# Performance work log

Hardware: AMD Instinct MI355X
Metric: run time of the kernel (lower is better)

Reference implementation:

```python
import jax, jax.numpy as jnp
import numpy as np

KERNEL = 7  # median blur window size (odd)


def setup_inputs() -> dict:
    key = jax.random.key(0)
    # NCHW image batch, values in [0,1) like normalized images
    img = jax.random.uniform(key, (8, 3, 512, 512), dtype=jnp.float32)
    return {"img": img}


def _median_blur(img, k):
    # Matches kornia.filters.median_blur: zero padding ('same'), then median
    # over the k*k window. k*k is odd so the exact middle of the sorted
    # window equals torch.median's lower median.
    pad = k // 2
    b, c, h, w = img.shape
    x = jnp.pad(img, ((0, 0), (0, 0), (pad, pad), (pad, pad)))  # zero pad
    # unfold: [B, C, k*k, H, W] — same materialization as kornia's conv2d
    # with binary one-hot kernels. Loop is over the fixed k*k = 49 taps.
    patches = jnp.stack(
        [x[:, :, i:i + h, j:j + w] for i in range(k) for j in range(k)],
        axis=2,
    )
    mid = (k * k) // 2
    return jnp.sort(patches, axis=2)[:, :, mid]  # [B, C, H, W]


def reference(img):
    return _median_blur(img, KERNEL)
```

## Files before the change

kernel.cpp:

```cpp
#include <hip/hip_runtime.h>
#include <utility>

#define IMG_H 512
#define IMG_W 512

typedef _Float16 h2 __attribute__((ext_vector_type(2)));

__device__ __forceinline__ h2 h2min(h2 a, h2 b) { return __builtin_elementwise_min(a, b); }
__device__ __forceinline__ h2 h2max(h2 a, h2 b) { return __builtin_elementwise_max(a, b); }

struct Op { int kind, a, b; };
constexpr int NSLOT = 352;
constexpr int MAXOPS = 4096;
struct Prog { Op ops[MAXOPS]; int n; int nphys; bool ok; };

constexpr int pow2ceil(int x) { int p = 1; while (p < x) p += p; return p; }

struct Builder {
    Op ops[MAXOPS] = {};
    int n = 0;
    bool pad[NSLOT] = {};
    bool init[NSLOT] = {};
    bool ok = true;

    constexpr void emit(int k, int a, int b) {
        if (n < MAXOPS) ops[n++] = Op{k, a, b}; else ok = false;
    }
    constexpr void load(int s, int c) { emit(2, s, c); pad[s] = false; init[s] = true; }
    constexpr void mov(int d, int s) {
        if (!init[s] || d == s) ok = false;
        emit(1, d, s); pad[d] = pad[s]; init[d] = true;
    }
    constexpr void mkpad(int s) { pad[s] = true; init[s] = true; }
    constexpr void ce_(int a, int b) {
        if (!init[a] || !init[b]) { ok = false; return; }
        if (pad[a] && pad[b]) return;
        if (!pad[a] && pad[b]) return;
        if (pad[a] && !pad[b]) {
            emit(1, a, b); pad[a] = false; pad[b] = true; return;
        }
        emit(0, a, b);
    }
    constexpr void maxin(int a, int b) {
        if (!init[a] || !init[b] || pad[a] || pad[b]) ok = false;
        emit(5, a, b);
    }
    constexpr void minin(int a, int b) {
        if (!init[a] || !init[b] || pad[a] || pad[b]) ok = false;
        emit(4, a, b);
    }
    constexpr void sort_run(int base, int len) {
        for (int p = 1; p < len; p += p)
            for (int k = p; k > 0; k /= 2)
                for (int j = k % p; j + k < len; j += k + k)
                    for (int i = 0; i < k; ++i)
                        if (i + j + k < len)
                            if ((i + j) / (p + p) == (i + j + k) / (p + p))
                                ce_(base + i + j, base + i + j + k);
    }
    constexpr void merge_stage(int base, int P) {
        int nn = 2 * P, p = P;
        for (int k = p; k > 0; k /= 2)
            for (int j = k % p; j + k < nn; j += k + k)
                for (int i = 0; i < k; ++i) {
                    int a = i + j, b = i + j + k;
                    if (b < nn && a / (p + p) == b / (p + p)) ce_(base + a, base + b);
                }
    }
    constexpr void load_col(int base, int c) {
        for (int r = 0; r < 7; ++r) load(base + r, c * 7 + r);
        sort_run(base, 7);
    }
    constexpr void place(int dst, int src, int len, int P) {
        for (int i = 0; i < len; ++i) mov(dst + i, src + i);
        for (int i = len; i < P; ++i) mkpad(dst + i);
    }
    constexpr void merge_to(int dst, int s1, int l1, int s2, int l2) {
        int P = pow2ceil(l1 > l2 ? l1 : l2);
        place(dst, s1, l1, P);
        place(dst + P, s2, l2, P);
        merge_stage(dst, P);
    }
    constexpr void select_med49(int T, int A, int B, int o) {
        for (int t = 0; t < 7; ++t) {
            mov(T + t, A + 17 + t);
            maxin(B + 6 - t, T + t);
        }
        mov(T + 7, A + 24);
        minin(T, T + 1); minin(T + 2, T + 3);
        minin(T + 4, T + 5); minin(T + 6, T + 7);
        minin(T, T + 2); minin(T + 4, T + 6);
        minin(T, T + 4);
        if (!init[T] || pad[T]) ok = false;
        emit(3, o, T);
    }
};

constexpr Prog build() {
    Builder b{};
    constexpr int M12 = 112, M34 = 128, M56 = 144, M78 = 160, M910 = 176, M1112 = 192;
    constexpr int C28A = 208, C28B = 240, C42 = 272, T0 = 336, T1 = 344;

    for (int c = 1; c <= 8; ++c) b.load_col(8 * c, c);
    b.merge_to(M34, 8 * 3, 7, 8 * 4, 7);
    b.merge_to(M56, 8 * 5, 7, 8 * 6, 7);
    b.merge_to(C28A, M34, 14, M56, 14);
    b.merge_to(M12, 8 * 1, 7, 8 * 2, 7);
    b.merge_to(M78, 8 * 7, 7, 8 * 8, 7);

    b.merge_to(C42, C28A, 28, M12, 14);
    b.load_col(8 * 0, 0);
    b.select_med49(T0, C42, 8 * 0, 0);
    b.select_med49(T1, C42, 8 * 7, 1);

    b.merge_to(C42, C28A, 28, M78, 14);
    b.load_col(8 * 9, 9);
    b.select_med49(T0, C42, 8 * 2, 2);
    b.select_med49(T1, C42, 8 * 9, 3);

    b.load_col(8 * 10, 10);
    b.merge_to(M910, 8 * 9, 7, 8 * 10, 7);
    b.merge_to(C28B, M78, 14, M910, 14);

    b.merge_to(C42, C28B, 28, M56, 14);
    b.select_med49(T0, C42, 8 * 4, 4);
    b.load_col(8 * 11, 11);
    b.select_med49(T1, C42, 8 * 11, 5);

    b.load_col(8 * 12, 12);
    b.merge_to(M1112, 8 * 11, 7, 8 * 12, 7);
    b.merge_to(C42, C28B, 28, M1112, 14);
    b.select_med49(T0, C42, 8 * 6, 6);
    b.load_col(8 * 13, 13);
    b.select_med49(T1, C42, 8 * 13, 7);

    Prog p{};
    bool needed[NSLOT] = {};
    int kindr[MAXOPS] = {};
    bool keep[MAXOPS] = {};
    for (int t = b.n - 1; t >= 0; --t) {
        Op o = b.ops[t];
        if (o.kind == 3) { keep[t] = true; kindr[t] = 3; needed[o.b] = true; }
        else if (o.kind == 0) {
            bool na = needed[o.a], nb = needed[o.b];
            if (na && nb)      { keep[t] = true; kindr[t] = 0; }
            else if (na)       { keep[t] = true; kindr[t] = 4; needed[o.b] = true; }
            else if (nb)       { keep[t] = true; kindr[t] = 5; needed[o.a] = true; }
        } else if (o.kind == 1) {
            if (needed[o.a]) { keep[t] = true; kindr[t] = 1; needed[o.a] = false; needed[o.b] = true; }
        } else if (o.kind == 2) {
            if (needed[o.a]) { keep[t] = true; kindr[t] = 2; needed[o.a] = false; }
        } else if (o.kind == 4) {
            if (needed[o.a]) { keep[t] = true; kindr[t] = 4; needed[o.b] = true; }
        } else if (o.kind == 5) {
            if (needed[o.b]) { keep[t] = true; kindr[t] = 5; needed[o.a] = true; }
        }
    }
    p.n = 0;
    for (int t = 0; t < b.n; ++t)
        if (keep[t]) { p.ops[p.n] = b.ops[t]; p.ops[p.n].kind = kindr[t]; ++p.n; }
    p.ok = b.ok;

    bool live[NSLOT] = {};
    bool lu_a[MAXOPS] = {};
    bool lu_b[MAXOPS] = {};
    for (int t = p.n - 1; t >= 0; --t) {
        Op o = p.ops[t];
        if (o.kind == 0 || o.kind == 4 || o.kind == 5) {
            lu_a[t] = !live[o.a]; lu_b[t] = !live[o.b];
        } else if (o.kind == 1 || o.kind == 3) {
            lu_b[t] = !live[o.b];
        }
        if (o.kind == 0) { live[o.a] = false; live[o.b] = false; }
        else if (o.kind == 1 || o.kind == 2 || o.kind == 4) live[o.a] = false;
        else if (o.kind == 5) live[o.b] = false;
        if (o.kind == 0 || o.kind == 4 || o.kind == 5) { live[o.a] = true; live[o.b] = true; }
        else if (o.kind == 1 || o.kind == 3) live[o.b] = true;
    }
    for (int t = 0; t < p.n; ++t) {
        Op o = p.ops[t];
        if (o.kind == 0 && (lu_a[t] || lu_b[t])) p.ok = false;
        if (o.kind == 4 && lu_a[t]) p.ok = false;
        if (o.kind == 5 && lu_b[t]) p.ok = false;
    }
    int phys[NSLOT] = {};
    bool bound[NSLOT] = {};
    int freelist[NSLOT] = {};
    int nfree = 0, nphys = 0;
    for (int t = 0; t < p.n; ++t) {
        Op o = p.ops[t];
        if (o.kind == 0) {
            if (!bound[o.a] || !bound[o.b]) p.ok = false;
            p.ops[t].a = phys[o.a]; p.ops[t].b = phys[o.b];
        } else if (o.kind == 4) {
            if (!bound[o.a] || !bound[o.b]) p.ok = false;
            p.ops[t].a = phys[o.a]; p.ops[t].b = phys[o.b];
            if (lu_b[t]) { freelist[nfree++] = phys[o.b]; bound[o.b] = false; }
        } else if (o.kind == 5) {
            if (!bound[o.a] || !bound[o.b]) p.ok = false;
            p.ops[t].a = phys[o.a]; p.ops[t].b = phys[o.b];
            if (lu_a[t]) { freelist[nfree++] = phys[o.a]; bound[o.a] = false; }
        } else if (o.kind == 1) {
            if (!bound[o.b]) p.ok = false;
            int pb = phys[o.b];
            p.ops[t].b = pb;
            if (lu_b[t]) { freelist[nfree++] = pb; bound[o.b] = false; }
            if (bound[o.a]) { freelist[nfree++] = phys[o.a]; bound[o.a] = false; }
            int pa = (nfree > 0) ? freelist[--nfree] : nphys++;
            phys[o.a] = pa; bound[o.a] = true;
            p.ops[t].a = pa;
        } else if (o.kind == 2) {
            if (bound[o.a]) { freelist[nfree++] = phys[o.a]; bound[o.a] = false; }
            int pa = (nfree > 0) ? freelist[--nfree] : nphys++;
            phys[o.a] = pa; bound[o.a] = true;
            p.ops[t].a = pa;
        } else {
            if (!bound[o.b]) p.ok = false;
            p.ops[t].b = phys[o.b];
            if (lu_b[t]) { freelist[nfree++] = phys[o.b]; bound[o.b] = false; }
        }
        if (nphys > NSLOT || nfree > NSLOT) p.ok = false;
    }
    p.nphys = nphys;
    return p;
}

constexpr Prog PROG = build();
static_assert(PROG.ok && PROG.n > 0 && PROG.n < 2000, "program build failed");
static_assert(PROG.nphys > 0 && PROG.nphys <= 192, "regalloc blew up");

template <int P>
__device__ __forceinline__ h2& vslot(h2* v0, h2* v1, h2* v2) {
    if constexpr (P < 64) return v0[P];
    else if constexpr (P < 128) return v1[P - 64];
    else return v2[P - 128];
}
template <int P>
__device__ __forceinline__ h2 cslot(const h2* c0, const h2* c1) {
    if constexpr (P < 49) return c0[P];
    else return c1[P - 49];
}

template <int I>
__device__ __forceinline__ void step(h2* v0, h2* v1, h2* v2,
                                     const h2* c0, const h2* c1, h2* med) {
    constexpr Op o = PROG.ops[I];
    if constexpr (o.kind == 0) {
        h2& A = vslot<o.a>(v0, v1, v2);
        h2& B = vslot<o.b>(v0, v1, v2);
        h2 lo = h2min(A, B);
        h2 hi = h2max(A, B);
        A = lo; B = hi;
    } else if constexpr (o.kind == 1) {
        vslot<o.a>(v0, v1, v2) = vslot<o.b>(v0, v1, v2);
    } else if constexpr (o.kind == 2) {
        vslot<o.a>(v0, v1, v2) = cslot<o.b>(c0, c1);
    } else if constexpr (o.kind == 3) {
        med[o.a] = vslot<o.b>(v0, v1, v2);
    } else if constexpr (o.kind == 4) {
        h2& A = vslot<o.a>(v0, v1, v2);
        h2& B = vslot<o.b>(v0, v1, v2);
        A = h2min(A, B);
    } else {
        h2& A = vslot<o.a>(v0, v1, v2);
        h2& B = vslot<o.b>(v0, v1, v2);
        B = h2max(A, B);
    }
}

template <size_t... Is>
__device__ __forceinline__ void run_all(h2* v0, h2* v1, h2* v2,
                                        const h2* c0, const h2* c1, h2* med,
                                        std::index_sequence<Is...>) {
    (step<(int)Is>(v0, v1, v2, c0, c1, med), ...);
}

__global__ __launch_bounds__(256, 2) void median7x7_kernel(
        const float* __restrict__ img, float* __restrict__ out) {
    const int bc = blockIdx.z;
    const int tx = threadIdx.x;
    const int ty = threadIdx.y;
    const int x0 = (blockIdx.x * 64 + tx) * 8;
    const int y  = (blockIdx.y * 4 + ty) * 2;

    const float* base = img + (size_t)bc * (IMG_H * IMG_W);
    const bool okl = (x0 >= 4);
    const bool okr = (x0 <= 496);
    const int xl = okl ? (x0 - 4) : 0;
    const int xr = okr ? (x0 + 8) : 504;

    h2 c0[49], c1[49];
    float prv[14];
#pragma unroll
    for (int r = 0; r < 8; ++r) {
        const int yy = y - 3 + r;
        float4 Q0, Q1, Q2, Q3;
        if ((unsigned)yy < IMG_H) {
            const float* rp = base + (size_t)yy * IMG_W;
            Q0 = *(const float4*)(rp + xl);
            Q1 = *(const float4*)(rp + x0);
            Q2 = *(const float4*)(rp + x0 + 4);
            Q3 = *(const float4*)(rp + xr);
        } else {
            Q0 = make_float4(0.f, 0.f, 0.f, 0.f); Q1 = Q0; Q2 = Q0; Q3 = Q0;
        }
        float cur[14];
        cur[0] = okl ? Q0.y : 0.f; cur[1] = okl ? Q0.z : 0.f; cur[2] = okl ? Q0.w : 0.f;
        cur[3] = Q1.x; cur[4] = Q1.y; cur[5] = Q1.z; cur[6] = Q1.w;
        cur[7] = Q2.x; cur[8] = Q2.y; cur[9] = Q2.z; cur[10] = Q2.w;
        cur[11] = okr ? Q3.x : 0.f; cur[12] = okr ? Q3.y : 0.f; cur[13] = okr ? Q3.z : 0.f;
        if (r > 0) {
#pragma unroll
            for (int c = 0; c < 14; ++c) {
                const int idx = c * 7 + (r - 1);
                h2 val = (h2)__builtin_amdgcn_cvt_pkrtz(prv[c], cur[c]);
                if (idx < 49) c0[idx] = val; else c1[idx - 49] = val;
            }
        }
#pragma unroll
        for (int c = 0; c < 14; ++c) prv[c] = cur[c];
    }

    h2 va[64], vb[64], vc[64];
    h2 med[8];
    run_all(va, vb, vc, c0, c1, med, std::make_index_sequence<(size_t)PROG.n>{});

    float* op = out + (size_t)bc * (IMG_H * IMG_W) + (size_t)y * IMG_W + x0;
    *(float4*)op = make_float4((float)med[0].x, (float)med[1].x,
                               (float)med[2].x, (float)med[3].x);
    *(float4*)(op + 4) = make_float4((float)med[4].x, (float)med[5].x,
                                     (float)med[6].x, (float)med[7].x);
    *(float4*)(op + IMG_W) = make_float4((float)med[0].y, (float)med[1].y,
                                         (float)med[2].y, (float)med[3].y);
    *(float4*)(op + IMG_W + 4) = make_float4((float)med[4].y, (float)med[5].y,
                                             (float)med[6].y, (float)med[7].y);
}

extern "C" void kernel_launch(void* const* d_in, const int* in_sizes, int n_in,
                              void* d_out, int out_size, void* d_ws, size_t ws_size,
                              hipStream_t stream) {
    const float* img = (const float*)d_in[0];
    float* out = (float*)d_out;
    dim3 grid(1, 64, 24);
    dim3 block(64, 4, 1);
    hipLaunchKernelGGL(median7x7_kernel, grid, block, 0, stream, img, out);
}
```

Baseline: 88.78 us.

## Rebuild median network builder with SSA virtual slots and pad-free merges

Reworks the compile-time sorting-network generator so every value is a fresh virtual slot (SSA style), with merges tracking padding by index remapping instead of physical pad slots and moves. The median selection step now uses a three-operand max into a new slot rather than copying then doing an in-place max. This removes many redundant register moves from the generated compare-exchange program. In exchange the virtual slot space grows and the register allocator may use more physical slots, up to 256, which risks higher VGPR pressure or spills.

```diff
diff --git a/kernel.cpp b/kernel.cpp
--- a/kernel.cpp
+++ b/kernel.cpp
@@ -9,130 +9,119 @@
 __device__ __forceinline__ h2 h2min(h2 a, h2 b) { return __builtin_elementwise_min(a, b); }
 __device__ __forceinline__ h2 h2max(h2 a, h2 b) { return __builtin_elementwise_max(a, b); }
 
-struct Op { int kind, a, b; };
-constexpr int NSLOT = 352;
+struct Op { int kind, a, b, c; };
+constexpr int NSLOT = 512;
 constexpr int MAXOPS = 4096;
 struct Prog { Op ops[MAXOPS]; int n; int nphys; bool ok; };
 
 constexpr int pow2ceil(int x) { int p = 1; while (p < x) p += p; return p; }
+
+struct Run { int s[48]; int len; };
 
 struct Builder {
     Op ops[MAXOPS] = {};
     int n = 0;
-    bool pad[NSLOT] = {};
-    bool init[NSLOT] = {};
+    int nv = 0;
     bool ok = true;
 
-    constexpr void emit(int k, int a, int b) {
-        if (n < MAXOPS) ops[n++] = Op{k, a, b}; else ok = false;
-    }
-    constexpr void load(int s, int c) { emit(2, s, c); pad[s] = false; init[s] = true; }
-    constexpr void mov(int d, int s) {
-        if (!init[s] || d == s) ok = false;
-        emit(1, d, s); pad[d] = pad[s]; init[d] = true;
-    }
-    constexpr void mkpad(int s) { pad[s] = true; init[s] = true; }
-    constexpr void ce_(int a, int b) {
-        if (!init[a] || !init[b]) { ok = false; return; }
-        if (pad[a] && pad[b]) return;
-        if (!pad[a] && pad[b]) return;
-        if (pad[a] && !pad[b]) {
-            emit(1, a, b); pad[a] = false; pad[b] = true; return;
-        }
-        emit(0, a, b);
-    }
-    constexpr void maxin(int a, int b) {
-        if (!init[a] || !init[b] || pad[a] || pad[b]) ok = false;
-        emit(5, a, b);
-    }
-    constexpr void minin(int a, int b) {
-        if (!init[a] || !init[b] || pad[a] || pad[b]) ok = false;
-        emit(4, a, b);
-    }
-    constexpr void sort_run(int base, int len) {
-        for (int p = 1; p < len; p += p)
+    constexpr void emit(int k, int a, int b, int c) {
+        if (n < MAXOPS) ops[n++] = Op{k, a, b, c}; else ok = false;
+    }
+    constexpr int fresh() {
+        if (nv < NSLOT) return nv++;
+        ok = false; return 0;
+    }
+    constexpr Run load_col(int c) {
+        Run r{}; r.len = 7;
+        for (int i = 0; i < 7; ++i) { r.s[i] = fresh(); emit(2, r.s[i], c * 7 + i, 0); }
+        for (int p = 1; p < 7; p += p)
             for (int k = p; k > 0; k /= 2)
-                for (int j = k % p; j + k < len; j += k + k)
+                for (int j = k % p; j + k < 7; j += k + k)
                     for (int i = 0; i < k; ++i)
-                        if (i + j + k < len)
-                            if ((i + j) / (p + p) == (i + j + k) / (p + p))
-                                ce_(base + i + j, base + i + j + k);
-    }
-    constexpr void merge_stage(int base, int P) {
-        int nn = 2 * P, p = P;
-        for (int k = p; k > 0; k /= 2)
-            for (int j = k % p; j + k < nn; j += k + k)
+                        if (i + j + k < 7 && (i + j) / (p + p) == (i + j + k) / (p + p))
+                            emit(0, r.s[i + j], r.s[i + j + k], 0);
+        return r;
+    }
+    constexpr Run copy(const Run& a) {
+        Run r{}; r.len = a.len;
+        for (int i = 0; i < a.len; ++i) { r.s[i] = fresh(); emit(1, r.s[i], a.s[i], 0); }
+        return r;
+    }
+    constexpr Run merge(const Run& A, const Run& B) {
+        int P = pow2ceil(A.len > B.len ? A.len : B.len);
+        if (A.len > P || B.len > P || 2 * P > 96) { ok = false; }
+        int map[96] = {};
+        for (int i = 0; i < 2 * P; ++i) map[i] = -1;
+        for (int i = 0; i < A.len; ++i) map[i] = A.s[i];
+        for (int i = 0; i < B.len; ++i) map[P + i] = B.s[i];
+        for (int k = P; k > 0; k /= 2)
+            for (int j = k % P; j + k < 2 * P; j += k + k)
                 for (int i = 0; i < k; ++i) {
-                    int a = i + j, b = i + j + k;
-                    if (b < nn && a / (p + p) == b / (p + p)) ce_(base + a, base + b);
+                    int x = i + j, y = i + j + k;
+                    int a = map[x], b = map[y];
+                    if (a >= 0 && b >= 0) emit(0, a, b, 0);
+                    else if (a < 0 && b >= 0) { map[x] = b; map[y] = -1; }
                 }
-    }
-    constexpr void load_col(int base, int c) {
-        for (int r = 0; r < 7; ++r) load(base + r, c * 7 + r);
-        sort_run(base, 7);
-    }
-    constexpr void place(int dst, int src, int len, int P) {
-        for (int i = 0; i < len; ++i) mov(dst + i, src + i);
-        for (int i = len; i < P; ++i) mkpad(dst + i);
-    }
-    constexpr void merge_to(int dst, int s1, int l1, int s2, int l2) {
-        int P = pow2ceil(l1 > l2 ? l1 : l2);
-        place(dst, s1, l1, P);
-        place(dst + P, s2, l2, P);
-        merge_stage(dst, P);
-    }
-    constexpr void select_med49(int T, int A, int B, int o) {
+        Run r{}; r.len = A.len + B.len;
+        for (int i = 0; i < r.len; ++i) { if (map[i] < 0) ok = false; r.s[i] = map[i]; }
+        for (int i = r.len; i < 2 * P; ++i) if (map[i] >= 0) ok = false;
+        return r;
+    }
+    constexpr void select49(const Run& A, const Run& B, int o) {
+        if (A.len != 42 || B.len != 7) ok = false;
+        int T[7] = {};
         for (int t = 0; t < 7; ++t) {
-            mov(T + t, A + 17 + t);
-            maxin(B + 6 - t, T + t);
-        }
-        mov(T + 7, A + 24);
-        minin(T, T + 1); minin(T + 2, T + 3);
-        minin(T + 4, T + 5); minin(T + 6, T + 7);
-        minin(T, T + 2); minin(T + 4, T + 6);
-        minin(T, T + 4);
-        if (!init[T] || pad[T]) ok = false;
-        emit(3, o, T);
+            T[t] = fresh();
+            emit(7, A.s[17 + t], B.s[6 - t], T[t]);
+        }
+        emit(4, T[0], T[1], 0); emit(4, T[2], T[3], 0);
+        emit(4, T[4], T[5], 0); emit(4, T[6], A.s[24], 0);
+        emit(4, T[0], T[2], 0); emit(4, T[4], T[6], 0);
+        emit(4, T[0], T[4], 0);
+        emit(3, o, T[0], 0);
     }
 };
 
 constexpr Prog build() {
     Builder b{};
-    constexpr int M12 = 112, M34 = 128, M56 = 144, M78 = 160, M910 = 176, M1112 = 192;
-    constexpr int C28A = 208, C28B = 240, C42 = 272, T0 = 336, T1 = 344;
-
-    for (int c = 1; c <= 8; ++c) b.load_col(8 * c, c);
-    b.merge_to(M34, 8 * 3, 7, 8 * 4, 7);
-    b.merge_to(M56, 8 * 5, 7, 8 * 6, 7);
-    b.merge_to(C28A, M34, 14, M56, 14);
-    b.merge_to(M12, 8 * 1, 7, 8 * 2, 7);
-    b.merge_to(M78, 8 * 7, 7, 8 * 8, 7);
-
-    b.merge_to(C42, C28A, 28, M12, 14);
-    b.load_col(8 * 0, 0);
-    b.select_med49(T0, C42, 8 * 0, 0);
-    b.select_med49(T1, C42, 8 * 7, 1);
-
-    b.merge_to(C42, C28A, 28, M78, 14);
-    b.load_col(8 * 9, 9);
-    b.select_med49(T0, C42, 8 * 2, 2);
-    b.select_med49(T1, C42, 8 * 9, 3);
-
-    b.load_col(8 * 10, 10);
-    b.merge_to(M910, 8 * 9, 7, 8 * 10, 7);
-    b.merge_to(C28B, M78, 14, M910, 14);
-
-    b.merge_to(C42, C28B, 28, M56, 14);
-    b.select_med49(T0, C42, 8 * 4, 4);
-    b.load_col(8 * 11, 11);
-    b.select_med49(T1, C42, 8 * 11, 5);
-
-    b.load_col(8 * 12, 12);
-    b.merge_to(M1112, 8 * 11, 7, 8 * 12, 7);
-    b.merge_to(C42, C28B, 28, M1112, 14);
-    b.select_med49(T0, C42, 8 * 6, 6);
-    b.load_col(8 * 13, 13);
-    b.select_med49(T1, C42, 8 * 13, 7);
+    Run g1 = b.load_col(1), g2 = b.load_col(2), g3 = b.load_col(3),
+        g4 = b.load_col(4), g5 = b.load_col(5), g6 = b.load_col(6),
+        g7 = b.load_col(7), g8 = b.load_col(8);
+    Run g2c = b.copy(g2), g4c = b.copy(g4), g6c = b.copy(g6);
+
+    Run M12 = b.merge(g1, g2c);
+    Run M34 = b.merge(g3, g4c);
+    Run M56 = b.merge(g5, g6c);
+    Run M56b = b.copy(M56);
+    Run C28A = b.merge(M34, M56);
+    Run C28Ac = b.copy(C28A);
+    Run C42A = b.merge(C28Ac, M12);
+    Run g0 = b.load_col(0);
+    b.select49(C42A, g0, 0);
+    b.select49(C42A, g7, 1);
+
+    Run M78 = b.merge(g7, g8);
+    Run M78b = b.copy(M78);
+    Run C42B = b.merge(C28A, M78);
+    Run g9 = b.load_col(9);
+    b.select49(C42B, g2, 2);
+    b.select49(C42B, g9, 3);
+
+    Run g10 = b.load_col(10);
+    Run M910 = b.merge(g9, g10);
+    Run C28B = b.merge(M78b, M910);
+    Run C28Bc = b.copy(C28B);
+    Run C42C = b.merge(C28Bc, M56b);
+    Run g11 = b.load_col(11);
+    b.select49(C42C, g4, 4);
+    b.select49(C42C, g11, 5);
+
+    Run g12 = b.load_col(12);
+    Run M1112 = b.merge(g11, g12);
+    Run C42D = b.merge(C28B, M1112);
+    Run g13 = b.load_col(13);
+    b.select49(C42D, g6, 6);
+    b.select49(C42D, g13, 7);
 
     Prog p{};
     bool needed[NSLOT] = {};
@@ -154,6 +143,9 @@
             if (needed[o.a]) { keep[t] = true; kindr[t] = 4; needed[o.b] = true; }
         } else if (o.kind == 5) {
             if (needed[o.b]) { keep[t] = true; kindr[t] = 5; needed[o.a] = true; }
+        } else if (o.kind == 7) {
+            if (needed[o.c]) { keep[t] = true; kindr[t] = 7; needed[o.c] = false;
+                               needed[o.a] = true; needed[o.b] = true; }
         }
     }
     p.n = 0;
@@ -166,7 +158,7 @@
     bool lu_b[MAXOPS] = {};
     for (int t = p.n - 1; t >= 0; --t) {
         Op o = p.ops[t];
-        if (o.kind == 0 || o.kind == 4 || o.kind == 5) {
+        if (o.kind == 0 || o.kind == 4 || o.kind == 5 || o.kind == 7) {
             lu_a[t] = !live[o.a]; lu_b[t] = !live[o.b];
         } else if (o.kind == 1 || o.kind == 3) {
             lu_b[t] = !live[o.b];
@@ -174,8 +166,10 @@
         if (o.kind == 0) { live[o.a] = false; live[o.b] = false; }
         else if (o.kind == 1 || o.kind == 2 || o.kind == 4) live[o.a] = false;
         else if (o.kind == 5) live[o.b] = false;
-        if (o.kind == 0 || o.kind == 4 || o.kind == 5) { live[o.a] = true; live[o.b] = true; }
-        else if (o.kind == 1 || o.kind == 3) live[o.b] = true;
+        else if (o.kind == 7) live[o.c] = false;
+        if (o.kind == 0 || o.kind == 4 || o.kind == 5 || o.kind == 7) {
+            live[o.a] = true; live[o.b] = true;
+        } else if (o.kind == 1 || o.kind == 3) live[o.b] = true;
     }
     for (int t = 0; t < p.n; ++t) {
         Op o = p.ops[t];
@@ -200,17 +194,23 @@
             if (!bound[o.a] || !bound[o.b]) p.ok = false;
             p.ops[t].a = phys[o.a]; p.ops[t].b = phys[o.b];
             if (lu_a[t]) { freelist[nfree++] = phys[o.a]; bound[o.a] = false; }
+        } else if (o.kind == 7) {
+            if (!bound[o.a] || !bound[o.b]) p.ok = false;
+            p.ops[t].a = phys[o.a]; p.ops[t].b = phys[o.b];
+            if (lu_a[t]) { freelist[nfree++] = phys[o.a]; bound[o.a] = false; }
+            if (lu_b[t]) { freelist[nfree++] = phys[o.b]; bound[o.b] = false; }
+            int pc = (nfree > 0) ? freelist[--nfree] : nphys++;
+            phys[o.c] = pc; bound[o.c] = true;
+            p.ops[t].c = pc;
         } else if (o.kind == 1) {
             if (!bound[o.b]) p.ok = false;
             int pb = phys[o.b];
             p.ops[t].b = pb;
             if (lu_b[t]) { freelist[nfree++] = pb; bound[o.b] = false; }
-            if (bound[o.a]) { freelist[nfree++] = phys[o.a]; bound[o.a] = false; }
             int pa = (nfree > 0) ? freelist[--nfree] : nphys++;
             phys[o.a] = pa; bound[o.a] = true;
             p.ops[t].a = pa;
         } else if (o.kind == 2) {
-            if (bound[o.a]) { freelist[nfree++] = phys[o.a]; bound[o.a] = false; }
             int pa = (nfree > 0) ? freelist[--nfree] : nphys++;
             phys[o.a] = pa; bound[o.a] = true;
             p.ops[t].a = pa;
@@ -226,14 +226,16 @@
 }
 
 constexpr Prog PROG = build();
-static_assert(PROG.ok && PROG.n > 0 && PROG.n < 2000, "program build failed");
-static_assert(PROG.nphys > 0 && PROG.nphys <= 192, "regalloc blew up");
+static_assert(PROG.ok, "program build failed");
+static_assert(PROG.n > 300 && PROG.n < 2400, "op count out of range");
+static_assert(PROG.nphys > 0 && PROG.nphys <= 256, "regalloc blew up");
 
 template <int P>
-__device__ __forceinline__ h2& vslot(h2* v0, h2* v1, h2* v2) {
+__device__ __forceinline__ h2& vslot(h2* v0, h2* v1, h2* v2, h2* v3) {
     if constexpr (P < 64) return v0[P];
     else if constexpr (P < 128) return v1[P - 64];
-    else return v2[P - 128];
+    else if constexpr (P < 192) return v2[P - 128];
+    else return v3[P - 192];
 }
 template <int P>
 __device__ __forceinline__ h2 cslot(const h2* c0, const h2* c1) {
@@ -242,37 +244,38 @@
 }
 
 template <int I>
-__device__ __forceinline__ void step(h2* v0, h2* v1, h2* v2,
+__device__ __forceinline__ void step(h2* v0, h2* v1, h2* v2, h2* v3,
                                      const h2* c0, const h2* c1, h2* med) {
     constexpr Op o = PROG.ops[I];
     if constexpr (o.kind == 0) {
-        h2& A = vslot<o.a>(v0, v1, v2);
-        h2& B = vslot<o.b>(v0, v1, v2);
+        h2& A = vslot<o.a>(v0, v1, v2, v3);
+        h2& B = vslot<o.b>(v0, v1, v2, v3);
         h2 lo = h2min(A, B);
         h2 hi = h2max(A, B);
         A = lo; B = hi;
     } else if constexpr (o.kind == 1) {
-        vslot<o.a>(v0, v1, v2) = vslot<o.b>(v0, v1, v2);
+        vslot<o.a>(v0, v1, v2, v3) = vslot<o.b>(v0, v1, v2, v3);
     } else if constexpr (o.kind == 2) {
-        vslot<o.a>(v0, v1, v2) = cslot<o.b>(c0, c1);
+        vslot<o.a>(v0, v1, v2, v3) = cslot<o.b>(c0, c1);
     } else if constexpr (o.kind == 3) {
-        med[o.a] = vslot<o.b>(v0, v1, v2);
+        med[o.a] = vslot<o.b>(v0, v1, v2, v3);
     } else if constexpr (o.kind == 4) {
-        h2& A = vslot<o.a>(v0, v1, v2);
-        h2& B = vslot<o.b>(v0, v1, v2);
-        A = h2min(A, B);
+        h2& A = vslot<o.a>(v0, v1, v2, v3);
+        A = h2min(A, vslot<o.b>(v0, v1, v2, v3));
+    } else if constexpr (o.kind == 5) {
+        h2& B = vslot<o.b>(v0, v1, v2, v3);
+        B = h2max(vslot<o.a>(v0, v1, v2, v3), B);
     } else {
-        h2& A = vslot<o.a>(v0, v1, v2);
-        h2& B = vslot<o.b>(v0, v1, v2);
-        B = h2max(A, B);
+        vslot<o.c>(v0, v1, v2, v3) =
+            h2max(vslot<o.a>(v0, v1, v2, v3), vslot<o.b>(v0, v1, v2, v3));
     }
 }
 
 template <size_t... Is>
-__device__ __forceinline__ void run_all(h2* v0, h2* v1, h2* v2,
+__device__ __forceinline__ void run_all(h2* v0, h2* v1, h2* v2, h2* v3,
                                         const h2* c0, const h2* c1, h2* med,
                                         std::index_sequence<Is...>) {
-    (step<(int)Is>(v0, v1, v2, c0, c1, med), ...);
+    (step<(int)Is>(v0, v1, v2, v3, c0, c1, med), ...);
 }
 
 __global__ __launch_bounds__(256, 2) void median7x7_kernel(
@@ -321,9 +324,9 @@
         for (int c = 0; c < 14; ++c) prv[c] = cur[c];
     }
 
-    h2 va[64], vb[64], vc[64];
+    h2 va[64], vb[64], vc[64], vd[64];
     h2 med[8];
-    run_all(va, vb, vc, c0, c1, med, std::make_index_sequence<(size_t)PROG.n>{});
+    run_all(va, vb, vc, vd, c0, c1, med, std::make_index_sequence<(size_t)PROG.n>{});
 
     float* op = out + (size_t)bc * (IMG_H * IMG_W) + (size_t)y * IMG_W + x0;
     *(float4*)op = make_float4((float)med[0].x, (float)med[1].x,
```

After: 89.08 us. No clear change (+0.3%).
